# Kernel tuning notes

Hardware: AMD Instinct MI355X
Metric: run time of the kernel (lower is better)

Reference implementation:

```python
import jax, jax.numpy as jnp
import numpy as np
import math

NDIM = 16
SCALE = math.sqrt(1.0 / NDIM)


def setup_inputs() -> dict:
    key = jax.random.key(0)
    ks = jax.random.split(key, 7)
    L, Bsz, Dm = 4096, 4, 1024
    return {
        "x": jax.random.normal(ks[0], (L, Bsz, Dm), dtype=jnp.float32),
        "log_dt": jax.random.normal(ks[1], (Dm, 1), dtype=jnp.float32),
        "log_A_real": jax.random.normal(ks[2], (Dm, NDIM), dtype=jnp.float32),
        "A_imag": jax.random.normal(ks[3], (Dm, NDIM), dtype=jnp.float32),
        "B": jax.random.normal(ks[4], (Dm, NDIM, 2), dtype=jnp.float32),
        "C": jax.random.normal(ks[5], (Dm, NDIM, 2), dtype=jnp.float32),
        "D_param": jax.random.normal(ks[6], (Dm,), dtype=jnp.float32),
    }


def _compute_kernel(log_dt, log_A_real, A_imag, B, C, length):
    dt = jnp.exp(log_dt)                                  # (D,1)
    A = -jnp.exp(log_A_real) + 1j * A_imag                # (D,N) complex
    dtA = A * dt                                          # (D,N)
    Cc = (B[..., 0] + 1j * B[..., 1]) * (C[..., 0] + 1j * C[..., 1])  # (D,N)
    # bilinear discretization
    p = Cc * dt / (1.0 - dtA / 2)                         # (D,N)
    log_q = jnp.log((1.0 + dtA / 2) / (1.0 - dtA / 2))    # (D,N)
    # Vandermonde: (D,N,L) complex — the kernel-gen bottleneck
    vander = jnp.exp(jnp.arange(length)[None, None, :] * log_q[:, :, None])
    k = jnp.einsum('dnl,dn->dl', vander, p * SCALE).real  # (D,L)
    return k


def reference(x, log_dt, log_A_real, A_imag, B, C, D_param):
    seq_len, bsz, dim = x.shape
    residual = x * D_param                                # (L,B,D)
    xt = jnp.transpose(x, (1, 2, 0))                      # (B,D,L)
    k = _compute_kernel(log_dt, log_A_real, A_imag, B, C, seq_len)
    fft_len = 2 * seq_len
    k_f = jnp.fft.rfft(k.astype(jnp.float32), n=fft_len)  # (D, fft_len//2+1)
    x_f = jnp.fft.rfft(xt.astype(jnp.float32), n=fft_len)  # (B,D, fft_len//2+1)
    out = jnp.fft.irfft(x_f * k_f, n=fft_len)[..., :seq_len]  # (B,D,L)
    out = out.astype(x.dtype)
    return jax.nn.silu(jnp.transpose(out, (2, 0, 1)) + residual)
```

## Files before the change

kernel.cpp:

```cpp
#include <hip/hip_runtime.h>
#include <math.h>

#define L_SEQ  4096
#define BSZ    4
#define DM     1024
#define NS     16
#define NSH    8
#define NV     (NSH / 2)
#define NCHUNK 64
#define CHUNK  (L_SEQ / NCHUNK)
#define LOG2_CHUNK 6
#define SCALE  0.25f
#define LBD    (BSZ * DM)

typedef float v2f __attribute__((ext_vector_type(2)));


__global__ void s4d_params(const float* __restrict__ log_dt,
                           const float* __restrict__ log_A_real,
                           const float* __restrict__ A_imag,
                           const float* __restrict__ Bp,
                           const float* __restrict__ Cp,
                           float2* __restrict__ qbuf,
                           float2* __restrict__ pbuf) {
    int t = blockIdx.x * blockDim.x + threadIdx.x;
    if (t >= NS * DM) return;
    int n = t >> 10, d = t & (DM - 1);
    int i = d * NS + n;
    float dt = expf(log_dt[d]);
    float Ar = -expf(log_A_real[i]);
    float Ai = A_imag[i];
    float ar = 0.5f * Ar * dt, ai = 0.5f * Ai * dt;
    float den_r = 1.0f - ar, den_i = -ai;
    float num_r = 1.0f + ar, num_i = ai;
    float inv = 1.0f / (den_r * den_r + den_i * den_i);
    float qr = (num_r * den_r + num_i * den_i) * inv;
    float qi = (num_i * den_r - num_r * den_i) * inv;
    float B0 = Bp[2 * i], B1 = Bp[2 * i + 1];
    float C0 = Cp[2 * i], C1 = Cp[2 * i + 1];
    float ccr = B0 * C0 - B1 * C1;
    float cci = B0 * C1 + B1 * C0;
    float s = dt * inv * SCALE;
    float pr = (ccr * den_r + cci * den_i) * s;
    float pi = (cci * den_r - ccr * den_i) * s;
    qbuf[t] = make_float2(qr, qi);
    pbuf[t] = make_float2(pr, pi);
}

__attribute__((amdgpu_waves_per_eu(4, 4)))
__global__ __launch_bounds__(256)
void s4d_pass1(const float* __restrict__ x,
               const float2* __restrict__ qbuf,
               float2* __restrict__ S) {
    int tid  = blockIdx.x * 256 + threadIdx.x;
    int lane = tid & 63;
    int dlo  = lane & 31;
    int half = lane >> 5;
    int u    = tid >> 6;
    int dhi  = u & 31;
    int bc   = u >> 5;
    int c    = bc & (NCHUNK - 1);
    int d    = dhi * 32 + dlo;
    int b    = bc >> LOG2_CHUNK;
    int nb   = half * NSH;

    v2f Qr[NV], Qi[NV], Hr[NV], Hi[NV];
#pragma unroll
    for (int k = 0; k < NV; ++k) {
        float2 a = qbuf[(nb + 2 * k) * DM + d];
        float2 bq = qbuf[(nb + 2 * k + 1) * DM + d];
        Qr[k] = (v2f){a.x, bq.x};
        Qi[k] = (v2f){a.y, bq.y};
        Hr[k] = (v2f){0.0f, 0.0f};
        Hi[k] = (v2f){0.0f, 0.0f};
    }
    const float* xp = x + (size_t)(c * CHUNK) * LBD + b * DM + d;
#pragma unroll
    for (int l0 = 0; l0 < CHUNK; l0 += 4) {
        float xv0 = xp[(size_t)(l0 + 0) * LBD];
        float xv1 = xp[(size_t)(l0 + 1) * LBD];
        float xv2 = xp[(size_t)(l0 + 2) * LBD];
        float xv3 = xp[(size_t)(l0 + 3) * LBD];
#define P1STEP(XV)                                                            \
        {                                                                     \
            v2f X = {XV, XV};                                                 \
            _Pragma("unroll")                                                 \
            for (int k = 0; k < NV; ++k) {                                    \
                v2f nr = __builtin_elementwise_fma(Qr[k], Hr[k],              \
                          __builtin_elementwise_fma(-Qi[k], Hi[k], X));       \
                v2f ni = __builtin_elementwise_fma(Qr[k], Hi[k],              \
                                                   Qi[k] * Hr[k]);            \
                Hr[k] = nr; Hi[k] = ni;                                       \
            }                                                                 \
        }
        P1STEP(xv0) P1STEP(xv1) P1STEP(xv2) P1STEP(xv3)
#undef P1STEP
    }
    float2* sp = S + ((size_t)bc * NS + nb) * DM + d;
#pragma unroll
    for (int k = 0; k < NV; ++k) {
        sp[(size_t)(2 * k) * DM]     = make_float2(Hr[k].x, Hi[k].x);
        sp[(size_t)(2 * k + 1) * DM] = make_float2(Hr[k].y, Hi[k].y);
    }
}

__global__ __launch_bounds__(256)
void s4d_pass2(const float2* __restrict__ qbuf,
               float2* __restrict__ S) {
    int tid = blockIdx.x * 256 + threadIdx.x;
    int d = tid & (DM - 1);
    int n = (tid >> 10) & (NS - 1);
    int b = tid >> 14;
    float2 qv = qbuf[n * DM + d];
    float qr = qv.x, qi = qv.y;
#pragma unroll
    for (int i = 0; i < LOG2_CHUNK; ++i) {
        float nr = qr * qr - qi * qi;
        float ni = 2.0f * qr * qi;
        qr = nr; qi = ni;
    }
    size_t base = ((size_t)b * NCHUNK * NS + n) * DM + d;
    const size_t cs = (size_t)NS * DM;
    float hr = 0.0f, hi = 0.0f;
    float2 s0 = S[base + 0 * cs], s1 = S[base + 1 * cs],
           s2 = S[base + 2 * cs], s3 = S[base + 3 * cs],
           s4 = S[base + 4 * cs], s5 = S[base + 5 * cs],
           s6 = S[base + 6 * cs], s7 = S[base + 7 * cs];
#pragma unroll
    for (int c0 = 0; c0 < NCHUNK; c0 += 8) {
        float2 t0, t1, t2, t3, t4, t5, t6, t7;
        if (c0 + 8 < NCHUNK) {
            size_t nb2 = base + (size_t)(c0 + 8) * cs;
            t0 = S[nb2 + 0 * cs]; t1 = S[nb2 + 1 * cs];
            t2 = S[nb2 + 2 * cs]; t3 = S[nb2 + 3 * cs];
            t4 = S[nb2 + 4 * cs]; t5 = S[nb2 + 5 * cs];
            t6 = S[nb2 + 6 * cs]; t7 = S[nb2 + 7 * cs];
        }
#define STEP(J, SB)                                                      \
        {                                                                \
            S[base + (size_t)(c0 + J) * cs] = make_float2(hr, hi);       \
            float nr = fmaf(qr, hr, fmaf(-qi, hi, SB.x));                \
            float ni = fmaf(qr, hi, fmaf(qi, hr, SB.y));                 \
            hr = nr; hi = ni;                                            \
        }
        STEP(0, s0) STEP(1, s1) STEP(2, s2) STEP(3, s3)
        STEP(4, s4) STEP(5, s5) STEP(6, s6) STEP(7, s7)
#undef STEP
        if (c0 + 8 < NCHUNK) {
            s0 = t0; s1 = t1; s2 = t2; s3 = t3;
            s4 = t4; s5 = t5; s6 = t6; s7 = t7;
        }
    }
}

__attribute__((amdgpu_waves_per_eu(4, 4)))
__global__ __launch_bounds__(256)
void s4d_pass3(const float* __restrict__ x,
               const float* __restrict__ Dp,
               const float2* __restrict__ qbuf,
               const float2* __restrict__ pbuf,
               const float2* __restrict__ S,
               float* __restrict__ out) {
    int tid  = blockIdx.x * 256 + threadIdx.x;
    int lane = tid & 63;
    int dlo  = lane & 31;
    int half = lane >> 5;
    int u    = tid >> 6;
    int dhi  = u & 31;
    int bc   = u >> 5;
    int c    = bc & (NCHUNK - 1);
    int d    = dhi * 32 + dlo;
    int b    = bc >> LOG2_CHUNK;
    int nb   = half * NSH;

    v2f Qr[NV], Qi[NV], Pr[NV], Pi[NV], Hr[NV], Hi[NV];
#pragma unroll
    for (int k = 0; k < NV; ++k) {
        float2 a0 = qbuf[(nb + 2 * k) * DM + d];
        float2 a1 = qbuf[(nb + 2 * k + 1) * DM + d];
        float2 w0 = pbuf[(nb + 2 * k) * DM + d];
        float2 w1 = pbuf[(nb + 2 * k + 1) * DM + d];
        Qr[k] = (v2f){a0.x, a1.x};
        Qi[k] = (v2f){a0.y, a1.y};
        Pr[k] = (v2f){w0.x, w1.x};
        Pi[k] = (v2f){w0.y, w1.y};
    }
    const float2* sp = S + ((size_t)bc * NS + nb) * DM + d;
#pragma unroll
    for (int k = 0; k < NV; ++k) {
        float2 s0 = sp[(size_t)(2 * k) * DM];
        float2 s1 = sp[(size_t)(2 * k + 1) * DM];
        Hr[k] = (v2f){s0.x, s1.x};
        Hi[k] = (v2f){s0.y, s1.y};
    }
    float dpar = Dp[d];
    const float* xp = x + (size_t)(c * CHUNK) * LBD + b * DM + d;
    float* op = out + (size_t)(c * CHUNK) * LBD + b * DM + d;
#pragma unroll
    for (int l0 = 0; l0 < CHUNK; l0 += 4) {
        float xv0 = xp[(size_t)(l0 + 0) * LBD];
        float xv1 = xp[(size_t)(l0 + 1) * LBD];
        float xv2 = xp[(size_t)(l0 + 2) * LBD];
        float xv3 = xp[(size_t)(l0 + 3) * LBD];
        float acc0, acc1, acc2, acc3;
#define P3STEP(XV, ACC)                                                       \
        {                                                                     \
            v2f X = {XV, XV};                                                 \
            v2f A = {0.0f, 0.0f};                                             \
            _Pragma("unroll")                                                 \
            for (int k = 0; k < NV; ++k) {                                    \
                v2f nr = __builtin_elementwise_fma(Qr[k], Hr[k],              \
                          __builtin_elementwise_fma(-Qi[k], Hi[k], X));       \
                v2f ni = __builtin_elementwise_fma(Qr[k], Hi[k],              \
                                                   Qi[k] * Hr[k]);            \
                Hr[k] = nr; Hi[k] = ni;                                       \
                A = __builtin_elementwise_fma(Pr[k], nr,                      \
                     __builtin_elementwise_fma(-Pi[k], ni, A));               \
            }                                                                 \
            ACC = A.x + A.y;                                                  \
        }
        P3STEP(xv0, acc0) P3STEP(xv1, acc1) P3STEP(xv2, acc2) P3STEP(xv3, acc3)
#undef P3STEP
        acc0 += __shfl_xor(acc0, 32, 64);
        acc1 += __shfl_xor(acc1, 32, 64);
        acc2 += __shfl_xor(acc2, 32, 64);
        acc3 += __shfl_xor(acc3, 32, 64);
        float z0 = fmaf(xv0, dpar, acc0);
        float z1 = fmaf(xv1, dpar, acc1);
        float z2 = fmaf(xv2, dpar, acc2);
        float z3 = fmaf(xv3, dpar, acc3);
        float r0 = z0 * __builtin_amdgcn_rcpf(1.0f + __expf(-z0));
        float r1 = z1 * __builtin_amdgcn_rcpf(1.0f + __expf(-z1));
        float r2 = z2 * __builtin_amdgcn_rcpf(1.0f + __expf(-z2));
        float r3 = z3 * __builtin_amdgcn_rcpf(1.0f + __expf(-z3));
        if (half == 0) {
            op[(size_t)(l0 + 0) * LBD] = r0;
            op[(size_t)(l0 + 1) * LBD] = r1;
            op[(size_t)(l0 + 2) * LBD] = r2;
            op[(size_t)(l0 + 3) * LBD] = r3;
        }
    }
}

extern "C" void kernel_launch(void* const* d_in, const int* in_sizes, int n_in,
                              void* d_out, int out_size, void* d_ws, size_t ws_size,
                              hipStream_t stream) {
    const float* x          = (const float*)d_in[0];
    const float* log_dt     = (const float*)d_in[1];
    const float* log_A_real = (const float*)d_in[2];
    const float* A_imag     = (const float*)d_in[3];
    const float* Bp         = (const float*)d_in[4];
    const float* Cp         = (const float*)d_in[5];
    const float* Dp         = (const float*)d_in[6];
    float* out = (float*)d_out;

    float2* qbuf = (float2*)d_ws;
    float2* pbuf = qbuf + NS * DM;
    float2* S    = pbuf + NS * DM;

    hipLaunchKernelGGL(s4d_params, dim3((NS * DM) / 256), dim3(256), 0, stream,
                       log_dt, log_A_real, A_imag, Bp, Cp, qbuf, pbuf);
    hipLaunchKernelGGL(s4d_pass1, dim3((2 * BSZ * NCHUNK * DM) / 256), dim3(256), 0, stream,
                       x, qbuf, S);
    hipLaunchKernelGGL(s4d_pass2, dim3((BSZ * DM * NS) / 256), dim3(256), 0, stream,
                       qbuf, S);
    hipLaunchKernelGGL(s4d_pass3, dim3((2 * BSZ * NCHUNK * DM) / 256), dim3(256), 0, stream,
                       x, Dp, qbuf, pbuf, S, out);
}
```

Baseline: 195.4 us.

## Split chunk-carry scan into two levels and double-buffer x loads

The serial 64-step inter-chunk carry scan becomes a two-level scan. The first kernel handles groups of 8 chunks in parallel and writes group totals. A small second kernel scans the 8 group totals. Pass3 then rebuilds each chunk's incoming state from its group prefix and local prefix, computing a power of q per chunk. Pass1 and pass3 also switch to double-buffered 8-wide x loads, and pass1's occupancy hint is raised. In exchange there is an extra launch, more workspace, and extra complex multiplies in pass3's prologue.

Result: no change. 193.9 us (-0.8%).

```diff
diff --git a/kernel.cpp b/kernel.cpp
--- a/kernel.cpp
+++ b/kernel.cpp
@@ -10,6 +10,8 @@
 #define NCHUNK 64
 #define CHUNK  (L_SEQ / NCHUNK)
 #define LOG2_CHUNK 6
+#define GRP    8
+#define NG     (NCHUNK / GRP)
 #define SCALE  0.25f
 #define LBD    (BSZ * DM)
 
@@ -47,7 +49,7 @@
     pbuf[t] = make_float2(pr, pi);
 }
 
-__attribute__((amdgpu_waves_per_eu(4, 4)))
+__attribute__((amdgpu_waves_per_eu(6, 8)))
 __global__ __launch_bounds__(256)
 void s4d_pass1(const float* __restrict__ x,
                const float2* __restrict__ qbuf,
@@ -75,27 +77,33 @@
         Hi[k] = (v2f){0.0f, 0.0f};
     }
     const float* xp = x + (size_t)(c * CHUNK) * LBD + b * DM + d;
-#pragma unroll
-    for (int l0 = 0; l0 < CHUNK; l0 += 4) {
-        float xv0 = xp[(size_t)(l0 + 0) * LBD];
-        float xv1 = xp[(size_t)(l0 + 1) * LBD];
-        float xv2 = xp[(size_t)(l0 + 2) * LBD];
-        float xv3 = xp[(size_t)(l0 + 3) * LBD];
-#define P1STEP(XV)                                                            \
-        {                                                                     \
-            v2f X = {XV, XV};                                                 \
-            _Pragma("unroll")                                                 \
-            for (int k = 0; k < NV; ++k) {                                    \
-                v2f nr = __builtin_elementwise_fma(Qr[k], Hr[k],              \
-                          __builtin_elementwise_fma(-Qi[k], Hi[k], X));       \
-                v2f ni = __builtin_elementwise_fma(Qr[k], Hi[k],              \
-                                                   Qi[k] * Hr[k]);            \
-                Hr[k] = nr; Hi[k] = ni;                                       \
-            }                                                                 \
-        }
-        P1STEP(xv0) P1STEP(xv1) P1STEP(xv2) P1STEP(xv3)
-#undef P1STEP
-    }
+    float xa[8], xb[8];
+#define LOADX(ARR, L0)                                                        \
+    { _Pragma("unroll")                                                       \
+      for (int j = 0; j < 8; ++j) ARR[j] = xp[(size_t)((L0) + j) * LBD]; }
+#define STEP1(XV)                                                             \
+    { v2f X = {XV, XV};                                                       \
+      _Pragma("unroll")                                                       \
+      for (int k = 0; k < NV; ++k) {                                          \
+          v2f nr = __builtin_elementwise_fma(Qr[k], Hr[k],                    \
+                    __builtin_elementwise_fma(-Qi[k], Hi[k], X));             \
+          v2f ni = __builtin_elementwise_fma(Qr[k], Hi[k], Qi[k] * Hr[k]);    \
+          Hr[k] = nr; Hi[k] = ni;                                             \
+      } }
+#define COMP1(ARR)                                                            \
+    { _Pragma("unroll")                                                       \
+      for (int j = 0; j < 8; ++j) STEP1(ARR[j]) }
+    LOADX(xa, 0)  LOADX(xb, 8)
+    COMP1(xa)     LOADX(xa, 16)
+    COMP1(xb)     LOADX(xb, 24)
+    COMP1(xa)     LOADX(xa, 32)
+    COMP1(xb)     LOADX(xb, 40)
+    COMP1(xa)     LOADX(xa, 48)
+    COMP1(xb)     LOADX(xb, 56)
+    COMP1(xa)
+    COMP1(xb)
+#undef COMP1
+#undef STEP1
     float2* sp = S + ((size_t)bc * NS + nb) * DM + d;
 #pragma unroll
     for (int k = 0; k < NV; ++k) {
@@ -105,8 +113,45 @@
 }
 
 __global__ __launch_bounds__(256)
-void s4d_pass2(const float2* __restrict__ qbuf,
-               float2* __restrict__ S) {
+void s4d_pass2a(const float2* __restrict__ qbuf,
+                float2* __restrict__ S,
+                float2* __restrict__ GT) {
+    int tid = blockIdx.x * 256 + threadIdx.x;
+    int d = tid & (DM - 1);
+    int n = (tid >> 10) & (NS - 1);
+    int g = (tid >> 14) & (NG - 1);
+    int b = tid >> 17;
+    float2 qv = qbuf[n * DM + d];
+    float qr = qv.x, qi = qv.y;
+#pragma unroll
+    for (int i = 0; i < LOG2_CHUNK; ++i) {
+        float nr = qr * qr - qi * qi;
+        float ni = 2.0f * qr * qi;
+        qr = nr; qi = ni;
+    }
+    size_t base = ((size_t)(b * NCHUNK + g * GRP) * NS + n) * DM + d;
+    const size_t cs = (size_t)NS * DM;
+    float2 s0 = S[base + 0 * cs], s1 = S[base + 1 * cs],
+           s2 = S[base + 2 * cs], s3 = S[base + 3 * cs],
+           s4 = S[base + 4 * cs], s5 = S[base + 5 * cs],
+           s6 = S[base + 6 * cs], s7 = S[base + 7 * cs];
+    float hr = 0.0f, hi = 0.0f;
+#define ST2(J, SB)                                                       \
+    {                                                                    \
+        S[base + (size_t)(J) * cs] = make_float2(hr, hi);                \
+        float nr = fmaf(qr, hr, fmaf(-qi, hi, SB.x));                    \
+        float ni = fmaf(qr, hi, fmaf(qi, hr, SB.y));                     \
+        hr = nr; hi = ni;                                                \
+    }
+    ST2(0, s0) ST2(1, s1) ST2(2, s2) ST2(3, s3)
+    ST2(4, s4) ST2(5, s5) ST2(6, s6) ST2(7, s7)
+#undef ST2
+    GT[((size_t)(b * NG + g) * NS + n) * DM + d] = make_float2(hr, hi);
+}
+
+__global__ __launch_bounds__(256)
+void s4d_pass2b(const float2* __restrict__ qbuf,
+                float2* __restrict__ GT) {
     int tid = blockIdx.x * 256 + threadIdx.x;
     int d = tid & (DM - 1);
     int n = (tid >> 10) & (NS - 1);
@@ -114,43 +159,28 @@
     float2 qv = qbuf[n * DM + d];
     float qr = qv.x, qi = qv.y;
 #pragma unroll
-    for (int i = 0; i < LOG2_CHUNK; ++i) {
+    for (int i = 0; i < LOG2_CHUNK + 3; ++i) {
         float nr = qr * qr - qi * qi;
         float ni = 2.0f * qr * qi;
         qr = nr; qi = ni;
     }
-    size_t base = ((size_t)b * NCHUNK * NS + n) * DM + d;
-    const size_t cs = (size_t)NS * DM;
+    size_t gbase = ((size_t)(b * NG) * NS + n) * DM + d;
+    const size_t gs = (size_t)NS * DM;
+    float2 t0 = GT[gbase + 0 * gs], t1 = GT[gbase + 1 * gs],
+           t2 = GT[gbase + 2 * gs], t3 = GT[gbase + 3 * gs],
+           t4 = GT[gbase + 4 * gs], t5 = GT[gbase + 5 * gs],
+           t6 = GT[gbase + 6 * gs], t7 = GT[gbase + 7 * gs];
     float hr = 0.0f, hi = 0.0f;
-    float2 s0 = S[base + 0 * cs], s1 = S[base + 1 * cs],
-           s2 = S[base + 2 * cs], s3 = S[base + 3 * cs],
-           s4 = S[base + 4 * cs], s5 = S[base + 5 * cs],
-           s6 = S[base + 6 * cs], s7 = S[base + 7 * cs];
-#pragma unroll
-    for (int c0 = 0; c0 < NCHUNK; c0 += 8) {
-        float2 t0, t1, t2, t3, t4, t5, t6, t7;
-        if (c0 + 8 < NCHUNK) {
-            size_t nb2 = base + (size_t)(c0 + 8) * cs;
-            t0 = S[nb2 + 0 * cs]; t1 = S[nb2 + 1 * cs];
-            t2 = S[nb2 + 2 * cs]; t3 = S[nb2 + 3 * cs];
-            t4 = S[nb2 + 4 * cs]; t5 = S[nb2 + 5 * cs];
-            t6 = S[nb2 + 6 * cs]; t7 = S[nb2 + 7 * cs];
-        }
-#define STEP(J, SB)                                                      \
-        {                                                                \
-            S[base + (size_t)(c0 + J) * cs] = make_float2(hr, hi);       \
-            float nr = fmaf(qr, hr, fmaf(-qi, hi, SB.x));                \
-            float ni = fmaf(qr, hi, fmaf(qi, hr, SB.y));                 \
-            hr = nr; hi = ni;                                            \
-        }
-        STEP(0, s0) STEP(1, s1) STEP(2, s2) STEP(3, s3)
-        STEP(4, s4) STEP(5, s5) STEP(6, s6) STEP(7, s7)
-#undef STEP
-        if (c0 + 8 < NCHUNK) {
-            s0 = t0; s1 = t1; s2 = t2; s3 = t3;
-            s4 = t4; s5 = t5; s6 = t6; s7 = t7;
-        }
-    }
+#define STB(J, SB)                                                       \
+    {                                                                    \
+        GT[gbase + (size_t)(J) * gs] = make_float2(hr, hi);              \
+        float nr = fmaf(qr, hr, fmaf(-qi, hi, SB.x));                    \
+        float ni = fmaf(qr, hi, fmaf(qi, hr, SB.y));                     \
+        hr = nr; hi = ni;                                                \
+    }
+    STB(0, t0) STB(1, t1) STB(2, t2) STB(3, t3)
+    STB(4, t4) STB(5, t5) STB(6, t6) STB(7, t7)
+#undef STB
 }
 
 __attribute__((amdgpu_waves_per_eu(4, 4)))
@@ -160,6 +190,7 @@
                const float2* __restrict__ qbuf,
                const float2* __restrict__ pbuf,
                const float2* __restrict__ S,
+               const float2* __restrict__ GT,
                float* __restrict__ out) {
     int tid  = blockIdx.x * 256 + threadIdx.x;
     int lane = tid & 63;
@@ -172,6 +203,8 @@
     int d    = dhi * 32 + dlo;
     int b    = bc >> LOG2_CHUNK;
     int nb   = half * NSH;
+    int g    = c >> 3;
+    int jj   = c & 7;
 
     v2f Qr[NV], Qi[NV], Pr[NV], Pi[NV], Hr[NV], Hi[NV];
 #pragma unroll
@@ -186,60 +219,92 @@
         Pi[k] = (v2f){w0.y, w1.y};
     }
     const float2* sp = S + ((size_t)bc * NS + nb) * DM + d;
+    const float2* gp = GT + ((size_t)(b * NG + g) * NS + nb) * DM + d;
 #pragma unroll
     for (int k = 0; k < NV; ++k) {
         float2 s0 = sp[(size_t)(2 * k) * DM];
         float2 s1 = sp[(size_t)(2 * k + 1) * DM];
-        Hr[k] = (v2f){s0.x, s1.x};
-        Hi[k] = (v2f){s0.y, s1.y};
+        float2 g0 = gp[(size_t)(2 * k) * DM];
+        float2 g1 = gp[(size_t)(2 * k + 1) * DM];
+        v2f Gr = (v2f){g0.x, g1.x};
+        v2f Gi = (v2f){g0.y, g1.y};
+        v2f ar = Qr[k], ai = Qi[k];
+#pragma unroll
+        for (int i = 0; i < LOG2_CHUNK; ++i) {
+            v2f nr = __builtin_elementwise_fma(-ai, ai, ar * ar);
+            v2f ni = (ar + ar) * ai;
+            ar = nr; ai = ni;
+        }
+        v2f wr = (v2f){1.0f, 1.0f}, wi = (v2f){0.0f, 0.0f};
+        if (jj & 1) {
+            v2f tr = __builtin_elementwise_fma(-wi, ai, wr * ar);
+            v2f ti = __builtin_elementwise_fma(wi, ar, wr * ai);
+            wr = tr; wi = ti;
+        }
+        { v2f nr = __builtin_elementwise_fma(-ai, ai, ar * ar);
+          v2f ni = (ar + ar) * ai; ar = nr; ai = ni; }
+        if (jj & 2) {
+            v2f tr = __builtin_elementwise_fma(-wi, ai, wr * ar);
+            v2f ti = __builtin_elementwise_fma(wi, ar, wr * ai);
+            wr = tr; wi = ti;
+        }
+        { v2f nr = __builtin_elementwise_fma(-ai, ai, ar * ar);
+          v2f ni = (ar + ar) * ai; ar = nr; ai = ni; }
+        if (jj & 4) {
+            v2f tr = __builtin_elementwise_fma(-wi, ai, wr * ar);
+            v2f ti = __builtin_elementwise_fma(wi, ar, wr * ai);
+            wr = tr; wi = ti;
+        }
+        v2f sr = (v2f){s0.x, s1.x};
+        v2f si = (v2f){s0.y, s1.y};
+        Hr[k] = __builtin_elementwise_fma(wr, Gr,
+                 __builtin_elementwise_fma(-wi, Gi, sr));
+        Hi[k] = __builtin_elementwise_fma(wr, Gi,
+                 __builtin_elementwise_fma(wi, Gr, si));
     }
     float dpar = Dp[d];
     const float* xp = x + (size_t)(c * CHUNK) * LBD + b * DM + d;
     float* op = out + (size_t)(c * CHUNK) * LBD + b * DM + d;
-#pragma unroll
-    for (int l0 = 0; l0 < CHUNK; l0 += 4) {
-        float xv0 = xp[(size_t)(l0 + 0) * LBD];
-        float xv1 = xp[(size_t)(l0 + 1) * LBD];
-        float xv2 = xp[(size_t)(l0 + 2) * LBD];
-        float xv3 = xp[(size_t)(l0 + 3) * LBD];
-        float acc0, acc1, acc2, acc3;
-#define P3STEP(XV, ACC)                                                       \
-        {                                                                     \
-            v2f X = {XV, XV};                                                 \
-            v2f A = {0.0f, 0.0f};                                             \
-            _Pragma("unroll")                                                 \
-            for (int k = 0; k < NV; ++k) {                                    \
-                v2f nr = __builtin_elementwise_fma(Qr[k], Hr[k],              \
-                          __builtin_elementwise_fma(-Qi[k], Hi[k], X));       \
-                v2f ni = __builtin_elementwise_fma(Qr[k], Hi[k],              \
-                                                   Qi[k] * Hr[k]);            \
-                Hr[k] = nr; Hi[k] = ni;                                       \
-                A = __builtin_elementwise_fma(Pr[k], nr,                      \
-                     __builtin_elementwise_fma(-Pi[k], ni, A));               \
-            }                                                                 \
-            ACC = A.x + A.y;                                                  \
-        }
-        P3STEP(xv0, acc0) P3STEP(xv1, acc1) P3STEP(xv2, acc2) P3STEP(xv3, acc3)
-#undef P3STEP
-        acc0 += __shfl_xor(acc0, 32, 64);
-        acc1 += __shfl_xor(acc1, 32, 64);
-        acc2 += __shfl_xor(acc2, 32, 64);
-        acc3 += __shfl_xor(acc3, 32, 64);
-        float z0 = fmaf(xv0, dpar, acc0);
-        float z1 = fmaf(xv1, dpar, acc1);
-        float z2 = fmaf(xv2, dpar, acc2);
-        float z3 = fmaf(xv3, dpar, acc3);
-        float r0 = z0 * __builtin_amdgcn_rcpf(1.0f + __expf(-z0));
-        float r1 = z1 * __builtin_amdgcn_rcpf(1.0f + __expf(-z1));
-        float r2 = z2 * __builtin_amdgcn_rcpf(1.0f + __expf(-z2));
-        float r3 = z3 * __builtin_amdgcn_rcpf(1.0f + __expf(-z3));
-        if (half == 0) {
-            op[(size_t)(l0 + 0) * LBD] = r0;
-            op[(size_t)(l0 + 1) * LBD] = r1;
-            op[(size_t)(l0 + 2) * LBD] = r2;
-            op[(size_t)(l0 + 3) * LBD] = r3;
-        }
-    }
+    float xa[8], xb[8];
+#define COMP3(ARR, L0)                                                        \
+    { float av[8];                                                            \
+      _Pragma("unroll")                                                       \
+      for (int j = 0; j < 8; ++j) {                                           \
+          v2f X = {ARR[j], ARR[j]};                                           \
+          v2f A = {0.0f, 0.0f};                                               \
+          _Pragma("unroll")                                                   \
+          for (int k = 0; k < NV; ++k) {                                      \
+              v2f nr = __builtin_elementwise_fma(Qr[k], Hr[k],                \
+                        __builtin_elementwise_fma(-Qi[k], Hi[k], X));         \
+              v2f ni = __builtin_elementwise_fma(Qr[k], Hi[k],                \
+                                                 Qi[k] * Hr[k]);              \
+              Hr[k] = nr; Hi[k] = ni;                                         \
+              A = __builtin_elementwise_fma(Pr[k], nr,                        \
+                   __builtin_elementwise_fma(-Pi[k], ni, A));                 \
+          }                                                                   \
+          av[j] = A.x + A.y;                                                  \
+      }                                                                       \
+      _Pragma("unroll")                                                       \
+      for (int j = 0; j < 8; ++j) av[j] += __shfl_xor(av[j], 32, 64);         \
+      if (half == 0) {                                                        \
+          _Pragma("unroll")                                                   \
+          for (int j = 0; j < 8; ++j) {                                       \
+              float z = fmaf(ARR[j], dpar, av[j]);                            \
+              float sg = __builtin_amdgcn_rcpf(1.0f + __expf(-z));            \
+              op[(size_t)((L0) + j) * LBD] = z * sg;                          \
+          }                                                                   \
+      } }
+    LOADX(xa, 0)  LOADX(xb, 8)
+    COMP3(xa, 0)  LOADX(xa, 16)
+    COMP3(xb, 8)  LOADX(xb, 24)
+    COMP3(xa, 16) LOADX(xa, 32)
+    COMP3(xb, 24) LOADX(xb, 40)
+    COMP3(xa, 32) LOADX(xa, 48)
+    COMP3(xb, 40) LOADX(xb, 56)
+    COMP3(xa, 48)
+    COMP3(xb, 56)
+#undef COMP3
+#undef LOADX
 }
 
 extern "C" void kernel_launch(void* const* d_in, const int* in_sizes, int n_in,
@@ -257,13 +322,16 @@
     float2* qbuf = (float2*)d_ws;
     float2* pbuf = qbuf + NS * DM;
     float2* S    = pbuf + NS * DM;
+    float2* GT   = S + (size_t)BSZ * NCHUNK * NS * DM;
 
     hipLaunchKernelGGL(s4d_params, dim3((NS * DM) / 256), dim3(256), 0, stream,
                        log_dt, log_A_real, A_imag, Bp, Cp, qbuf, pbuf);
     hipLaunchKernelGGL(s4d_pass1, dim3((2 * BSZ * NCHUNK * DM) / 256), dim3(256), 0, stream,
                        x, qbuf, S);
-    hipLaunchKernelGGL(s4d_pass2, dim3((BSZ * DM * NS) / 256), dim3(256), 0, stream,
-                       qbuf, S);
+    hipLaunchKernelGGL(s4d_pass2a, dim3((BSZ * NG * NS * DM) / 256), dim3(256), 0, stream,
+                       qbuf, S, GT);
+    hipLaunchKernelGGL(s4d_pass2b, dim3((BSZ * NS * DM) / 256), dim3(256), 0, stream,
+                       qbuf, GT);
     hipLaunchKernelGGL(s4d_pass3, dim3((2 * BSZ * NCHUNK * DM) / 256), dim3(256), 0, stream,
-                       x, Dp, qbuf, pbuf, S, out);
-}
+                       x, Dp, qbuf, pbuf, S, GT, out);
+}
```
